# Optimization experiments

Hardware: AMD Instinct MI355X
Metric: run time of the kernel (lower is better)

Reference implementation:

```python
import jax, jax.numpy as jnp
import numpy as np

N, A, D_IN, H, S = 4096, 256, 39, 50, 8


def setup_inputs() -> dict:
    key = jax.random.key(0)
    ks = jax.random.split(key, 8)
    sc1 = 1.0 / np.sqrt(D_IN)
    sc2 = 1.0 / np.sqrt(H)
    return {
        "desc": jax.random.normal(ks[0], (N, A, D_IN), dtype=jnp.float32),
        "numbers": jax.random.randint(ks[1], (A,), 0, S),
        "W1": jax.random.normal(ks[2], (S, D_IN, H), dtype=jnp.float32) * sc1,
        "b1": jax.random.normal(ks[3], (S, H), dtype=jnp.float32) * sc1,
        "W2": jax.random.normal(ks[4], (S, H, H), dtype=jnp.float32) * sc2,
        "b2": jax.random.normal(ks[5], (S, H), dtype=jnp.float32) * sc2,
        "W3": jax.random.normal(ks[6], (S, H, 1), dtype=jnp.float32) * sc2,
        "b3": jax.random.normal(ks[7], (S, 1), dtype=jnp.float32) * sc2,
    }


def reference(desc, numbers, W1, b1, W2, b2, W3, b3):
    # Species-routed per-atom MLP dispatch, vectorized by gathering each
    # atom's expert parameters (replaces the Python loop over ModuleDict).
    w1 = W1[numbers]            # [A, D_IN, H]
    w2 = W2[numbers]            # [A, H, H]
    w3 = W3[numbers]            # [A, H, 1]
    h = jax.nn.silu(jnp.einsum('nad,adh->nah', desc, w1) + b1[numbers])
    h = jax.nn.silu(jnp.einsum('nah,ahk->nak', h, w2) + b2[numbers])
    out = jnp.einsum('nah,aho->nao', h, w3) + b3[numbers]
    return out[..., 0]          # [N, A], matches tc.cat(temp, axis=1)
```

## Files before the change

### kernel.cpp

```cpp
#include <hip/hip_runtime.h>
#include <hip/hip_bf16.h>
#include <cstring>


#define NN    4096
#define AA    256
#define DIN   39
#define HH    50
#define ATILE 4
#define NTILE 64
#define XSTR  56
#define WFS   (2 * 2 * 4 * 64 * 8)

typedef __attribute__((ext_vector_type(8))) short bf16x8;
typedef __attribute__((ext_vector_type(4))) float f32x4;

__device__ __forceinline__ float fast_silu(float x) {
    return x * __builtin_amdgcn_rcpf(1.0f + __expf(-x));
}
__device__ __forceinline__ unsigned pack_bf2(float a, float b) {
    __hip_bfloat162 h = __float22bfloat162_rn(float2{a, b});
    unsigned u; memcpy(&u, &h, 4); return u;
}
__device__ __forceinline__ unsigned short bf16b(float a) {
    __hip_bfloat16 h = __float2bfloat16(a);
    unsigned short u; memcpy(&u, &h, 2); return u;
}

__global__ __launch_bounds__(256) void prep_weights(
    const float* __restrict__ W1, const float* __restrict__ b1,
    const float* __restrict__ W2, const float* __restrict__ b2,
    const float* __restrict__ W3, const float* __restrict__ b3,
    unsigned short* __restrict__ Wf, float* __restrict__ Bp)
{
    const int s = blockIdx.x >> 3;
    const int c = blockIdx.x & 7;
    const int t = threadIdx.x;
    const float* __restrict__ w1g = W1 + s * (DIN * HH);
    const float* __restrict__ w2g = W2 + s * (HH * HH);
    unsigned* __restrict__ outw = (unsigned*)(Wf + (size_t)s * WFS);

    #pragma unroll
    for (int i = 0; i < 2; ++i) {
        const int d    = c * 512 + i * 256 + t;
        const int j2   = d & 3;
        const int lane = (d >> 2) & 63;
        const int nf   = (d >> 8) & 3;
        const int ks   = (d >> 10) & 1;
        const int L    = (d >> 11) & 1;
        const int col  = 16 * nf + (lane & 15);
        const int k0   = ks * 32 + 8 * (lane >> 4) + 2 * j2;
        const int k1   = k0 + 1;
        float v0 = 0.f, v1 = 0.f;
        if (col < HH) {
            if (L == 0) {
                if (k0 < DIN) v0 = w1g[k0 * HH + col];
                if (k1 < DIN) v1 = w1g[k1 * HH + col];
            } else {
                if (k0 < HH)  v0 = w2g[k0 * HH + col];
                if (k1 < HH)  v1 = w2g[k1 * HH + col];
            }
        }
        outw[d] = pack_bf2(v0, v1);
    }
    if (c == 0 && t < 64) {
        float* bp = Bp + s * 256;
        const bool v = t < HH;
        bp[t]       = v ? b1[s * HH + t] : 0.0f;
        bp[64 + t]  = v ? b2[s * HH + t] : 0.0f;
        bp[128 + t] = v ? W3[s * HH + t] : 0.0f;
        bp[192 + t] = b3[s];
    }
}

__global__ __launch_bounds__(256, 4) void atomic_mlp_mfma(
    const float* __restrict__ desc,
    const int*   __restrict__ numbers,
    const unsigned short* __restrict__ Wf,
    const float* __restrict__ Bp,
    float*       __restrict__ out)
{
    __shared__ unsigned short Xb[ATILE * NTILE * XSTR + 8];
    __shared__ float          Ob[ATILE * NTILE];

    const int a0 = blockIdx.x * ATILE;
    const int n0 = blockIdx.y * NTILE;
    const int t  = threadIdx.x;

    #pragma unroll
    for (int i = 0; i < 10; ++i) {
        const int idx = t + 256 * i;
        if (idx < NTILE * 39) {
            const int seg = idx / 39;
            const int off = idx - 39 * seg;
            const float4 v = *(const float4*)(desc +
                ((size_t)(n0 + seg) * AA + a0) * DIN + off * 4);
            const int f0 = off * 4;
            #pragma unroll
            for (int j = 0; j < 4; ++j) {
                const int f  = f0 + j;
                const int at = f / 39;
                const int d  = f - 39 * at;
                Xb[(at * NTILE + seg) * XSTR + d] = bf16b(((const float*)&v)[j]);
            }
        }
    }
    Xb[t * XSTR + 39] = 0;
    *(uint4*)&Xb[t * XSTR + 40] = uint4{0u, 0u, 0u, 0u};
    *(uint4*)&Xb[t * XSTR + 48] = uint4{0u, 0u, 0u, 0u};
    if (t == 0) *(uint4*)&Xb[ATILE * NTILE * XSTR] = uint4{0u, 0u, 0u, 0u};

    const int lane = t & 63;
    const int lg   = lane >> 4;
    const int lr   = lane & 15;
    const int wid  = t >> 6;
    const int wbase = wid * NTILE;

    const int sw = __builtin_amdgcn_readfirstlane(numbers[a0 + wid]);
    const unsigned short* __restrict__ wfs = Wf + (size_t)sw * WFS;

    bf16x8 w1f[2][4], w2f[2][4];
    #pragma unroll
    for (int ks = 0; ks < 2; ++ks)
        #pragma unroll
        for (int nf = 0; nf < 4; ++nf) {
            w1f[ks][nf] = *(const bf16x8*)&wfs[((ks * 4 + nf) * 64 + lane) * 8];
            w2f[ks][nf] = *(const bf16x8*)&wfs[((8 + ks * 4 + nf) * 64 + lane) * 8];
        }

    const float* __restrict__ bp = Bp + sw * 256;
    float b1v[4], b2v[4], w3v[4];
    #pragma unroll
    for (int nf = 0; nf < 4; ++nf) {
        const int col = 16 * nf + lr;
        b1v[nf] = bp[col];
        b2v[nf] = bp[64 + col];
        w3v[nf] = bp[128 + col];
    }
    const float bias3 = bp[192];

    __syncthreads();

    #pragma unroll
    for (int mf = 0; mf < 4; ++mf) {
        const int rbase = wbase + 16 * mf;
        bf16x8 af0 = *(const bf16x8*)&Xb[(rbase + lr) * XSTR + 8 * lg];
        bf16x8 af1 = *(const bf16x8*)&Xb[(rbase + lr) * XSTR + 32 + 8 * lg];
        f32x4 a1[4];
        #pragma unroll
        for (int nf = 0; nf < 4; ++nf) a1[nf] = f32x4{0.f, 0.f, 0.f, 0.f};
        #pragma unroll
        for (int nf = 0; nf < 4; ++nf)
            a1[nf] = __builtin_amdgcn_mfma_f32_16x16x32_bf16(af0, w1f[0][nf], a1[nf], 0, 0, 0);
        #pragma unroll
        for (int nf = 0; nf < 4; ++nf)
            a1[nf] = __builtin_amdgcn_mfma_f32_16x16x32_bf16(af1, w1f[1][nf], a1[nf], 0, 0, 0);
        #pragma unroll
        for (int nf = 0; nf < 4; ++nf) {
            const int col = 16 * nf + lr;
            if (col < HH) {
                #pragma unroll
                for (int r = 0; r < 4; ++r)
                    Xb[(rbase + 4 * lg + r) * XSTR + col] =
                        bf16b(fast_silu(a1[nf][r] + b1v[nf]));
            }
        }
    }

    #pragma unroll
    for (int mf = 0; mf < 4; ++mf) {
        const int rbase = wbase + 16 * mf;
        bf16x8 af0 = *(const bf16x8*)&Xb[(rbase + lr) * XSTR + 8 * lg];
        bf16x8 af1 = *(const bf16x8*)&Xb[(rbase + lr) * XSTR + 32 + 8 * lg];
        f32x4 a2[4];
        #pragma unroll
        for (int nf = 0; nf < 4; ++nf) a2[nf] = f32x4{0.f, 0.f, 0.f, 0.f};
        #pragma unroll
        for (int nf = 0; nf < 4; ++nf)
            a2[nf] = __builtin_amdgcn_mfma_f32_16x16x32_bf16(af0, w2f[0][nf], a2[nf], 0, 0, 0);
        #pragma unroll
        for (int nf = 0; nf < 4; ++nf)
            a2[nf] = __builtin_amdgcn_mfma_f32_16x16x32_bf16(af1, w2f[1][nf], a2[nf], 0, 0, 0);

        float p0 = 0.f, p1 = 0.f, p2 = 0.f, p3 = 0.f;
        #pragma unroll
        for (int nf = 0; nf < 4; ++nf) {
            p0 += fast_silu(a2[nf][0] + b2v[nf]) * w3v[nf];
            p1 += fast_silu(a2[nf][1] + b2v[nf]) * w3v[nf];
            p2 += fast_silu(a2[nf][2] + b2v[nf]) * w3v[nf];
            p3 += fast_silu(a2[nf][3] + b2v[nf]) * w3v[nf];
        }
        #pragma unroll
        for (int off = 1; off < 16; off <<= 1) {
            p0 += __shfl_xor(p0, off);
            p1 += __shfl_xor(p1, off);
            p2 += __shfl_xor(p2, off);
            p3 += __shfl_xor(p3, off);
        }
        if (lr < 4) {
            const float pv = (lr == 0) ? p0 : (lr == 1) ? p1 : (lr == 2) ? p2 : p3;
            Ob[wbase + 16 * mf + 4 * lg + lr] = pv + bias3;
        }
    }

    __syncthreads();

    if (t < NTILE) {
        float4 o;
        o.x = Ob[0 * NTILE + t];
        o.y = Ob[1 * NTILE + t];
        o.z = Ob[2 * NTILE + t];
        o.w = Ob[3 * NTILE + t];
        *(float4*)&out[(size_t)(n0 + t) * AA + a0] = o;
    }
}

extern "C" void kernel_launch(void* const* d_in, const int* in_sizes, int n_in,
                              void* d_out, int out_size, void* d_ws, size_t ws_size,
                              hipStream_t stream) {
    const float* desc    = (const float*)d_in[0];
    const int*   numbers = (const int*)  d_in[1];
    const float* W1      = (const float*)d_in[2];
    const float* b1      = (const float*)d_in[3];
    const float* W2      = (const float*)d_in[4];
    const float* b2      = (const float*)d_in[5];
    const float* W3      = (const float*)d_in[6];
    const float* b3      = (const float*)d_in[7];
    float*       out     = (float*)d_out;

    unsigned short* Wf = (unsigned short*)d_ws;
    float*          Bp = (float*)((char*)d_ws + 8 * WFS * 2);

    hipLaunchKernelGGL(prep_weights, dim3(64), dim3(256), 0, stream,
                       W1, b1, W2, b2, W3, b3, Wf, Bp);

    dim3 grid(AA / ATILE, NN / NTILE);
    hipLaunchKernelGGL(atomic_mlp_mfma, grid, dim3(256), 0, stream,
                       desc, numbers, Wf, Bp, out);
}
```

Measured before the change: 71.28 us.

## Swap MFMA operand roles to compute transposed hidden tiles and shrink reductions

The MFMA operands are swapped so weights act as A and activations as B, producing transposed tiles where each lane holds four consecutive hidden units for one sample row. This allows packed 8-byte LDS stores of layer-1 activations instead of scalar 2-byte stores. The final layer-3 dot product then needs only two cross-lane shuffles instead of four rounds on four values. Bias and W3 vectors are now read per tile as float4 from global memory rather than held in registers, which adds loads but reduces register pressure.

```diff
diff --git a/kernel.cpp b/kernel.cpp
--- a/kernel.cpp
+++ b/kernel.cpp
@@ -45,10 +45,10 @@
         const int d    = c * 512 + i * 256 + t;
         const int j2   = d & 3;
         const int lane = (d >> 2) & 63;
-        const int nf   = (d >> 8) & 3;
+        const int mt   = (d >> 8) & 3;
         const int ks   = (d >> 10) & 1;
         const int L    = (d >> 11) & 1;
-        const int col  = 16 * nf + (lane & 15);
+        const int col  = 16 * mt + (lane & 15);
         const int k0   = ks * 32 + 8 * (lane >> 4) + 2 * j2;
         const int k1   = k0 + 1;
         float v0 = 0.f, v1 = 0.f;
@@ -123,84 +123,59 @@
     #pragma unroll
     for (int ks = 0; ks < 2; ++ks)
         #pragma unroll
-        for (int nf = 0; nf < 4; ++nf) {
-            w1f[ks][nf] = *(const bf16x8*)&wfs[((ks * 4 + nf) * 64 + lane) * 8];
-            w2f[ks][nf] = *(const bf16x8*)&wfs[((8 + ks * 4 + nf) * 64 + lane) * 8];
+        for (int mt = 0; mt < 4; ++mt) {
+            w1f[ks][mt] = *(const bf16x8*)&wfs[((ks * 4 + mt) * 64 + lane) * 8];
+            w2f[ks][mt] = *(const bf16x8*)&wfs[((8 + ks * 4 + mt) * 64 + lane) * 8];
         }
 
     const float* __restrict__ bp = Bp + sw * 256;
-    float b1v[4], b2v[4], w3v[4];
-    #pragma unroll
-    for (int nf = 0; nf < 4; ++nf) {
-        const int col = 16 * nf + lr;
-        b1v[nf] = bp[col];
-        b2v[nf] = bp[64 + col];
-        w3v[nf] = bp[128 + col];
-    }
     const float bias3 = bp[192];
 
     __syncthreads();
 
     #pragma unroll
-    for (int mf = 0; mf < 4; ++mf) {
-        const int rbase = wbase + 16 * mf;
-        bf16x8 af0 = *(const bf16x8*)&Xb[(rbase + lr) * XSTR + 8 * lg];
-        bf16x8 af1 = *(const bf16x8*)&Xb[(rbase + lr) * XSTR + 32 + 8 * lg];
-        f32x4 a1[4];
+    for (int nt = 0; nt < 4; ++nt) {
+        const int row = wbase + 16 * nt + lr;
+        bf16x8 xf0 = *(const bf16x8*)&Xb[row * XSTR + 8 * lg];
+        bf16x8 xf1 = *(const bf16x8*)&Xb[row * XSTR + 32 + 8 * lg];
         #pragma unroll
-        for (int nf = 0; nf < 4; ++nf) a1[nf] = f32x4{0.f, 0.f, 0.f, 0.f};
+        for (int mt = 0; mt < 4; ++mt) {
+            f32x4 cAcc = f32x4{0.f, 0.f, 0.f, 0.f};
+            cAcc = __builtin_amdgcn_mfma_f32_16x16x32_bf16(w1f[0][mt], xf0, cAcc, 0, 0, 0);
+            cAcc = __builtin_amdgcn_mfma_f32_16x16x32_bf16(w1f[1][mt], xf1, cAcc, 0, 0, 0);
+            const float4 b1q = *(const float4*)&bp[16 * mt + 4 * lg];
+            const unsigned u0 = pack_bf2(fast_silu(cAcc[0] + b1q.x),
+                                         fast_silu(cAcc[1] + b1q.y));
+            const unsigned u1 = pack_bf2(fast_silu(cAcc[2] + b1q.z),
+                                         fast_silu(cAcc[3] + b1q.w));
+            if (mt < 3 || lg < 2) {
+                uint2 uu; uu.x = u0; uu.y = u1;
+                *(uint2*)&Xb[row * XSTR + 16 * mt + 4 * lg] = uu;
+            }
+        }
+    }
+
+    #pragma unroll
+    for (int nt = 0; nt < 4; ++nt) {
+        const int row = wbase + 16 * nt + lr;
+        bf16x8 hf0 = *(const bf16x8*)&Xb[row * XSTR + 8 * lg];
+        bf16x8 hf1 = *(const bf16x8*)&Xb[row * XSTR + 32 + 8 * lg];
+        float p = 0.f;
         #pragma unroll
-        for (int nf = 0; nf < 4; ++nf)
-            a1[nf] = __builtin_amdgcn_mfma_f32_16x16x32_bf16(af0, w1f[0][nf], a1[nf], 0, 0, 0);
-        #pragma unroll
-        for (int nf = 0; nf < 4; ++nf)
-            a1[nf] = __builtin_amdgcn_mfma_f32_16x16x32_bf16(af1, w1f[1][nf], a1[nf], 0, 0, 0);
-        #pragma unroll
-        for (int nf = 0; nf < 4; ++nf) {
-            const int col = 16 * nf + lr;
-            if (col < HH) {
-                #pragma unroll
-                for (int r = 0; r < 4; ++r)
-                    Xb[(rbase + 4 * lg + r) * XSTR + col] =
-                        bf16b(fast_silu(a1[nf][r] + b1v[nf]));
-            }
-        }
-    }
-
-    #pragma unroll
-    for (int mf = 0; mf < 4; ++mf) {
-        const int rbase = wbase + 16 * mf;
-        bf16x8 af0 = *(const bf16x8*)&Xb[(rbase + lr) * XSTR + 8 * lg];
-        bf16x8 af1 = *(const bf16x8*)&Xb[(rbase + lr) * XSTR + 32 + 8 * lg];
-        f32x4 a2[4];
-        #pragma unroll
-        for (int nf = 0; nf < 4; ++nf) a2[nf] = f32x4{0.f, 0.f, 0.f, 0.f};
-        #pragma unroll
-        for (int nf = 0; nf < 4; ++nf)
-            a2[nf] = __builtin_amdgcn_mfma_f32_16x16x32_bf16(af0, w2f[0][nf], a2[nf], 0, 0, 0);
-        #pragma unroll
-        for (int nf = 0; nf < 4; ++nf)
-            a2[nf] = __builtin_amdgcn_mfma_f32_16x16x32_bf16(af1, w2f[1][nf], a2[nf], 0, 0, 0);
-
-        float p0 = 0.f, p1 = 0.f, p2 = 0.f, p3 = 0.f;
-        #pragma unroll
-        for (int nf = 0; nf < 4; ++nf) {
-            p0 += fast_silu(a2[nf][0] + b2v[nf]) * w3v[nf];
-            p1 += fast_silu(a2[nf][1] + b2v[nf]) * w3v[nf];
-            p2 += fast_silu(a2[nf][2] + b2v[nf]) * w3v[nf];
-            p3 += fast_silu(a2[nf][3] + b2v[nf]) * w3v[nf];
-        }
-        #pragma unroll
-        for (int off = 1; off < 16; off <<= 1) {
-            p0 += __shfl_xor(p0, off);
-            p1 += __shfl_xor(p1, off);
-            p2 += __shfl_xor(p2, off);
-            p3 += __shfl_xor(p3, off);
-        }
-        if (lr < 4) {
-            const float pv = (lr == 0) ? p0 : (lr == 1) ? p1 : (lr == 2) ? p2 : p3;
-            Ob[wbase + 16 * mf + 4 * lg + lr] = pv + bias3;
-        }
+        for (int mt = 0; mt < 4; ++mt) {
+            f32x4 cAcc = f32x4{0.f, 0.f, 0.f, 0.f};
+            cAcc = __builtin_amdgcn_mfma_f32_16x16x32_bf16(w2f[0][mt], hf0, cAcc, 0, 0, 0);
+            cAcc = __builtin_amdgcn_mfma_f32_16x16x32_bf16(w2f[1][mt], hf1, cAcc, 0, 0, 0);
+            const float4 b2q = *(const float4*)&bp[64 + 16 * mt + 4 * lg];
+            const float4 w3q = *(const float4*)&bp[128 + 16 * mt + 4 * lg];
+            p += fast_silu(cAcc[0] + b2q.x) * w3q.x;
+            p += fast_silu(cAcc[1] + b2q.y) * w3q.y;
+            p += fast_silu(cAcc[2] + b2q.z) * w3q.z;
+            p += fast_silu(cAcc[3] + b2q.w) * w3q.w;
+        }
+        p += __shfl_xor(p, 16);
+        p += __shfl_xor(p, 32);
+        if (lg == 0) Ob[wbase + 16 * nt + lr] = p + bias3;
     }
 
     __syncthreads();
```

Result: slower. 75.66 us (+6.1%).
